# Performance work log

Hardware: AMD Instinct MI355X
Metric: run time of the kernel (lower is better)

Reference implementation:

```python
import jax, jax.numpy as jnp
import numpy as np

B, L, DIM, NH = 2, 2048, 1024, 16
HD = DIM // NH

def setup_inputs() -> dict:
    key = jax.random.key(0)
    ks = jax.random.split(key, 7)
    s = 1.0 / np.sqrt(DIM)
    x = jax.random.normal(ks[0], (B, L, DIM), dtype=jnp.float32)
    pos_bias = jax.random.normal(ks[1], (B, NH, L, L), dtype=jnp.float32)
    mask = jax.random.randint(ks[2], (B, L), 0, 2, dtype=jnp.int32)
    wq = jax.random.normal(ks[3], (DIM, DIM), dtype=jnp.float32) * s
    wk = jax.random.normal(ks[4], (DIM, DIM), dtype=jnp.float32) * s
    wv = jax.random.normal(ks[5], (DIM, DIM), dtype=jnp.float32) * s
    wo = jax.random.normal(ks[6], (DIM, DIM), dtype=jnp.float32) * s
    return {"x": x, "pos_bias": pos_bias, "mask": mask, "wq": wq, "wk": wk, "wv": wv, "wo": wo}

def reference(x, pos_bias, mask, wq, wk, wv, wo):
    b, l, _ = x.shape
    # projections (bias-free linears); reshape to [B, L, n, c]
    q = (x @ wq).reshape(b, l, NH, HD)
    k = (x @ wk).reshape(b, l, NH, HD)
    v = (x @ wv).reshape(b, l, NH, HD)
    # additive bias: pos_bias, with masked positions set to dtype min (T5: no 1/sqrt(d) scaling)
    neg = jnp.finfo(x.dtype).min
    attn_bias = jnp.where(mask[:, None, None, :] == 0, neg, pos_bias)
    scores = jnp.einsum('binc,bjnc->bnij', q, k) + attn_bias  # [B, n, L, L]
    attn = jax.nn.softmax(scores, axis=-1)
    out = jnp.einsum('bnij,bjnc->binc', attn, v).reshape(b, l, DIM)
    return out @ wo
```

## Files before the change

### kernel.cpp

```cpp
#include <hip/hip_runtime.h>
#include <cmath>

typedef _Float16 half8 __attribute__((ext_vector_type(8)));
typedef _Float16 half4 __attribute__((ext_vector_type(4)));
typedef float f32x4 __attribute__((ext_vector_type(4)));

#define NEGBIG (-3.4028235e38f)

__global__ void cast4_kernel(const float* __restrict__ in, _Float16* __restrict__ out, int n) {
    int i = (blockIdx.x * 256 + threadIdx.x) * 4;
    if (i < n) {
        float4 v = *(const float4*)&in[i];
        half4 o = { (_Float16)v.x, (_Float16)v.y, (_Float16)v.z, (_Float16)v.w };
        *(half4*)&out[i] = o;
    }
}

__global__ void transpose_cast_kernel(const float* __restrict__ W, _Float16* __restrict__ Wt) {
    __shared__ float tile[32][33];
    int bx = blockIdx.x * 32;
    int by = blockIdx.y * 32;
    int tx = threadIdx.x & 31, ty = threadIdx.x >> 5;
    #pragma unroll
    for (int r = 0; r < 32; r += 8)
        tile[ty + r][tx] = W[(size_t)(bx + ty + r) * 1024 + by + tx];
    __syncthreads();
    #pragma unroll
    for (int r = 0; r < 32; r += 8)
        Wt[(size_t)(by + ty + r) * 1024 + bx + tx] = (_Float16)tile[tx][ty + r];
}

__global__ __launch_bounds__(256)
void gemm_qkv_kernel(const _Float16* __restrict__ X,
                     const _Float16* __restrict__ WqT, const _Float16* __restrict__ WkT,
                     const _Float16* __restrict__ WvT,
                     _Float16* __restrict__ Qh, _Float16* __restrict__ Kh, _Float16* __restrict__ VTh)
{
    const int z = blockIdx.z;
    const _Float16* __restrict__ Bt = (z == 0) ? WqT : (z == 1) ? WkT : WvT;
    _Float16* __restrict__ out      = (z == 0) ? Qh  : (z == 1) ? Kh  : VTh;

    __shared__ _Float16 Asb[128][40];
    __shared__ _Float16 Bsb[128][40];

    const int tid = threadIdx.x;
    const int bm = blockIdx.x * 128;
    const int bn = blockIdx.y * 128;
    const int wave = tid >> 6, lane = tid & 63;
    const int wm = (wave >> 1) * 64, wn = (wave & 1) * 64;
    const int quad = lane >> 4, l16 = lane & 15;

    f32x4 acc[4][4] = {};

    for (int k0 = 0; k0 < 1024; k0 += 32) {
        #pragma unroll
        for (int c = 0; c < 2; ++c) {
            int chunk = tid + c * 256;
            int row = chunk >> 2;
            int kc  = (chunk & 3) * 8;
            *(half8*)&Asb[row][kc] = *(const half8*)&X [(size_t)(bm + row) * 1024 + k0 + kc];
            *(half8*)&Bsb[row][kc] = *(const half8*)&Bt[(size_t)(bn + row) * 1024 + k0 + kc];
        }
        __syncthreads();
        half8 af[4], bf[4];
        #pragma unroll
        for (int mt = 0; mt < 4; ++mt) af[mt] = *(const half8*)&Asb[wm + mt*16 + l16][quad * 8];
        #pragma unroll
        for (int nt = 0; nt < 4; ++nt) bf[nt] = *(const half8*)&Bsb[wn + nt*16 + l16][quad * 8];
        if (z == 2) {
            #pragma unroll
            for (int mt = 0; mt < 4; ++mt)
                #pragma unroll
                for (int nt = 0; nt < 4; ++nt)
                    acc[mt][nt] = __builtin_amdgcn_mfma_f32_16x16x32_f16(bf[nt], af[mt], acc[mt][nt], 0, 0, 0);
        } else {
            #pragma unroll
            for (int mt = 0; mt < 4; ++mt)
                #pragma unroll
                for (int nt = 0; nt < 4; ++nt)
                    acc[mt][nt] = __builtin_amdgcn_mfma_f32_16x16x32_f16(af[mt], bf[nt], acc[mt][nt], 0, 0, 0);
        }
        __syncthreads();
    }

    if (z < 2) {
        #pragma unroll
        for (int mt = 0; mt < 4; ++mt) {
            #pragma unroll
            for (int nt = 0; nt < 4; ++nt) {
                #pragma unroll
                for (int r = 0; r < 4; ++r) {
                    int m = bm + wm + mt * 16 + quad * 4 + r;
                    int n = bn + wn + nt * 16 + l16;
                    _Float16 hv = (_Float16)acc[mt][nt][r];
                    int bb = m >> 11, ll = m & 2047, hh = n >> 6, dd = n & 63;
                    out[(((size_t)(bb * 16 + hh)) * 2048 + ll) * 64 + dd] = hv;
                }
            }
        }
    } else {
        #pragma unroll
        for (int mt = 0; mt < 4; ++mt) {
            #pragma unroll
            for (int nt = 0; nt < 4; ++nt) {
                #pragma unroll
                for (int r = 0; r < 4; ++r) {
                    int n = bn + wn + nt * 16 + quad * 4 + r;
                    int m = bm + wm + mt * 16 + l16;
                    _Float16 hv = (_Float16)acc[mt][nt][r];
                    int bb = m >> 11, ll = m & 2047, hh = n >> 6, dd = n & 63;
                    out[(((size_t)(bb * 16 + hh)) * 64 + dd) * 2048 + ll] = hv;
                }
            }
        }
    }
}

__device__ __forceinline__ float rowmax16(float v) {
    #pragma unroll
    for (int off = 1; off < 16; off <<= 1) v = fmaxf(v, __shfl_xor(v, off));
    return v;
}
__device__ __forceinline__ float rowsum16(float v) {
    #pragma unroll
    for (int off = 1; off < 16; off <<= 1) v += __shfl_xor(v, off);
    return v;
}

__global__ __launch_bounds__(256)
void flash_attn_kernel(const _Float16* __restrict__ Qh, const _Float16* __restrict__ Kh,
                       const _Float16* __restrict__ VTh, const float* __restrict__ bias,
                       const int* __restrict__ mask, _Float16* __restrict__ AO)
{
    const int qt = blockIdx.x, h = blockIdx.y, b = blockIdx.z;
    const int tid = threadIdx.x, wave = tid >> 6, lane = tid & 63;
    const int quad = lane >> 4, l16 = lane & 15;

    __shared__ _Float16 Kt[64][72];
    __shared__ _Float16 Vt[64][72];
    __shared__ float    Bs[64][68];
    __shared__ _Float16 Pw[4][16][72];

    const size_t head = (size_t)(b * 16 + h) * 2048 * 64;
    const int i_base = qt * 64 + wave * 16;
    const float* __restrict__ bias_base = bias + ((size_t)((b * 16 + h) * 2048 + qt * 64)) * 2048;
    const int* __restrict__ mask_base = mask + b * 2048;

    half8 qf0 = *(const half8*)&Qh[head + (size_t)(i_base + l16) * 64 + quad * 8];
    half8 qf1 = *(const half8*)&Qh[head + (size_t)(i_base + l16) * 64 + 32 + quad * 8];

    float m_r[4] = { -INFINITY, -INFINITY, -INFINITY, -INFINITY };
    float l_r[4] = {};
    f32x4 o[4] = {};

    const int kv_row = tid >> 3;
    const int kv_dc  = (tid & 7) * 8;
    const int b_row0 = tid >> 4;
    const int b_col  = (tid & 15) * 4;

    half8 kreg[2], vreg[2];
    f32x4 breg[4];
    int4  mreg;

    auto prefetch = [&](int j0) {
        #pragma unroll
        for (int c = 0; c < 2; ++c) {
            int row = kv_row + c * 32;
            kreg[c] = *(const half8*)&Kh [head + (size_t)(j0 + row) * 64 + kv_dc];
            vreg[c] = *(const half8*)&VTh[head + (size_t)row * 2048 + j0 + kv_dc];
        }
        mreg = *(const int4*)&mask_base[j0 + b_col];
        #pragma unroll
        for (int c = 0; c < 4; ++c)
            breg[c] = *(const f32x4*)&bias_base[(size_t)(b_row0 + c * 16) * 2048 + j0 + b_col];
    };

    prefetch(0);

    for (int j0 = 0; j0 < 2048; j0 += 64) {
        #pragma unroll
        for (int c = 0; c < 2; ++c) {
            int row = kv_row + c * 32;
            *(half8*)&Kt[row][kv_dc] = kreg[c];
            *(half8*)&Vt[row][kv_dc] = vreg[c];
        }
        #pragma unroll
        for (int c = 0; c < 4; ++c) {
            float* dst = &Bs[b_row0 + c * 16][b_col];
            dst[0] = mreg.x ? breg[c][0] : NEGBIG;
            dst[1] = mreg.y ? breg[c][1] : NEGBIG;
            dst[2] = mreg.z ? breg[c][2] : NEGBIG;
            dst[3] = mreg.w ? breg[c][3] : NEGBIG;
        }
        __syncthreads();

        if (j0 + 64 < 2048) prefetch(j0 + 64);

        const int iw = wave * 16 + quad * 4;
        float sreg[4][4];
        #pragma unroll
        for (int jt = 0; jt < 4; ++jt) {
            half8 kf0 = *(const half8*)&Kt[jt * 16 + l16][quad * 8];
            half8 kf1 = *(const half8*)&Kt[jt * 16 + l16][32 + quad * 8];
            f32x4 s = {};
            __builtin_amdgcn_s_setprio(1);
            s = __builtin_amdgcn_mfma_f32_16x16x32_f16(qf0, kf0, s, 0, 0, 0);
            s = __builtin_amdgcn_mfma_f32_16x16x32_f16(qf1, kf1, s, 0, 0, 0);
            __builtin_amdgcn_s_setprio(0);
            #pragma unroll
            for (int r = 0; r < 4; ++r)
                sreg[jt][r] = s[r] + Bs[iw + r][jt * 16 + l16];
        }

        float alpha[4];
        #pragma unroll
        for (int r = 0; r < 4; ++r) {
            float mx = fmaxf(fmaxf(sreg[0][r], sreg[1][r]), fmaxf(sreg[2][r], sreg[3][r]));
            mx = rowmax16(mx);
            float mnew = fmaxf(m_r[r], mx);
            alpha[r] = __expf(m_r[r] - mnew);
            m_r[r] = mnew;
            float ps = 0.f;
            #pragma unroll
            for (int jt = 0; jt < 4; ++jt) {
                float p = __expf(sreg[jt][r] - mnew);
                Pw[wave][quad * 4 + r][jt * 16 + l16] = (_Float16)p;
                ps += p;
            }
            ps = rowsum16(ps);
            l_r[r] = l_r[r] * alpha[r] + ps;
        }
        #pragma unroll
        for (int nt = 0; nt < 4; ++nt)
            #pragma unroll
            for (int r = 0; r < 4; ++r)
                o[nt][r] *= alpha[r];

        half8 pf0 = *(const half8*)&Pw[wave][l16][quad * 8];
        half8 pf1 = *(const half8*)&Pw[wave][l16][32 + quad * 8];
        #pragma unroll
        for (int nt = 0; nt < 4; ++nt) {
            half8 vf0 = *(const half8*)&Vt[nt * 16 + l16][quad * 8];
            half8 vf1 = *(const half8*)&Vt[nt * 16 + l16][32 + quad * 8];
            __builtin_amdgcn_s_setprio(1);
            o[nt] = __builtin_amdgcn_mfma_f32_16x16x32_f16(pf0, vf0, o[nt], 0, 0, 0);
            o[nt] = __builtin_amdgcn_mfma_f32_16x16x32_f16(pf1, vf1, o[nt], 0, 0, 0);
            __builtin_amdgcn_s_setprio(0);
        }
        __syncthreads();
    }

    #pragma unroll
    for (int nt = 0; nt < 4; ++nt) {
        #pragma unroll
        for (int r = 0; r < 4; ++r) {
            float val = o[nt][r] / l_r[r];
            AO[(size_t)(b * 2048 + i_base + quad * 4 + r) * 1024 + h * 64 + nt * 16 + l16] = (_Float16)val;
        }
    }
}

__global__ __launch_bounds__(256)
void gemm_out_kernel(const _Float16* __restrict__ A, const _Float16* __restrict__ Bt,
                     float* __restrict__ C)
{
    __shared__ _Float16 Asb[128][40];
    __shared__ _Float16 Bsb[128][40];

    const int tid = threadIdx.x;
    const int bm = blockIdx.x * 128;
    const int bn = blockIdx.y * 128;
    const int wave = tid >> 6, lane = tid & 63;
    const int wm = (wave >> 1) * 64, wn = (wave & 1) * 64;
    const int quad = lane >> 4, l16 = lane & 15;

    f32x4 acc[4][4] = {};

    for (int k0 = 0; k0 < 1024; k0 += 32) {
        #pragma unroll
        for (int c = 0; c < 2; ++c) {
            int chunk = tid + c * 256;
            int row = chunk >> 2;
            int kc  = (chunk & 3) * 8;
            *(half8*)&Asb[row][kc] = *(const half8*)&A [(size_t)(bm + row) * 1024 + k0 + kc];
            *(half8*)&Bsb[row][kc] = *(const half8*)&Bt[(size_t)(bn + row) * 1024 + k0 + kc];
        }
        __syncthreads();
        half8 af[4], bf[4];
        #pragma unroll
        for (int mt = 0; mt < 4; ++mt) af[mt] = *(const half8*)&Asb[wm + mt*16 + l16][quad * 8];
        #pragma unroll
        for (int nt = 0; nt < 4; ++nt) bf[nt] = *(const half8*)&Bsb[wn + nt*16 + l16][quad * 8];
        #pragma unroll
        for (int mt = 0; mt < 4; ++mt)
            #pragma unroll
            for (int nt = 0; nt < 4; ++nt)
                acc[mt][nt] = __builtin_amdgcn_mfma_f32_16x16x32_f16(af[mt], bf[nt], acc[mt][nt], 0, 0, 0);
        __syncthreads();
    }

    #pragma unroll
    for (int mt = 0; mt < 4; ++mt)
        #pragma unroll
        for (int nt = 0; nt < 4; ++nt)
            #pragma unroll
            for (int r = 0; r < 4; ++r) {
                int m = bm + wm + mt * 16 + quad * 4 + r;
                int n = bn + wn + nt * 16 + l16;
                C[(size_t)m * 1024 + n] = acc[mt][nt][r];
            }
}

extern "C" void kernel_launch(void* const* d_in, const int* in_sizes, int n_in,
                              void* d_out, int out_size, void* d_ws, size_t ws_size,
                              hipStream_t stream)
{
    const float* x    = (const float*)d_in[0];
    const float* bias = (const float*)d_in[1];
    const int*   mask = (const int*)d_in[2];
    const float* wq   = (const float*)d_in[3];
    const float* wk   = (const float*)d_in[4];
    const float* wv   = (const float*)d_in[5];
    const float* wo   = (const float*)d_in[6];
    float* out = (float*)d_out;

    char* ws = (char*)d_ws;
    const size_t MB = 1024 * 1024;
    _Float16* x_h = (_Float16*)(ws + 0);
    _Float16* AO  = x_h;
    _Float16* wqT = (_Float16*)(ws + 8 * MB);
    _Float16* wkT = (_Float16*)(ws + 10 * MB);
    _Float16* wvT = (_Float16*)(ws + 12 * MB);
    _Float16* woT = (_Float16*)(ws + 14 * MB);
    _Float16* Qh  = (_Float16*)(ws + 16 * MB);
    _Float16* Kh  = (_Float16*)(ws + 24 * MB);
    _Float16* VTh = (_Float16*)(ws + 32 * MB);

    cast4_kernel<<<4096, 256, 0, stream>>>(x, x_h, 4096 * 1024);
    dim3 tg(32, 32);
    transpose_cast_kernel<<<tg, 256, 0, stream>>>(wq, wqT);
    transpose_cast_kernel<<<tg, 256, 0, stream>>>(wk, wkT);
    transpose_cast_kernel<<<tg, 256, 0, stream>>>(wv, wvT);
    transpose_cast_kernel<<<tg, 256, 0, stream>>>(wo, woT);

    gemm_qkv_kernel<<<dim3(32, 8, 3), 256, 0, stream>>>(x_h, wqT, wkT, wvT, Qh, Kh, VTh);
    flash_attn_kernel<<<dim3(32, 16, 2), 256, 0, stream>>>(Qh, Kh, VTh, bias, mask, AO);
    gemm_out_kernel<<<dim3(32, 8), 256, 0, stream>>>(AO, woT, out);
}
```

Baseline: 846.4 us.

## Transpose attention MFMA layout, read bias in registers, use direct-to-LDS GEMM loads

The attention kernel swaps the MFMA operand order so each lane holds one query row's scores. Bias and mask are then loaded straight into registers instead of being staged through shared memory, and the row max and sum reductions shrink to two cross-lane shuffles. Both GEMMs now use global_load_lds to copy tiles directly into unpadded shared memory, and the four weight transpose launches are merged into one. The unpadded LDS tiles may cause bank conflicts, and the GEMM loop still synchronizes on every tile without double buffering.

```diff
diff --git a/kernel.cpp b/kernel.cpp
--- a/kernel.cpp
+++ b/kernel.cpp
@@ -6,6 +6,11 @@
 typedef float f32x4 __attribute__((ext_vector_type(4)));
 
 #define NEGBIG (-3.4028235e38f)
+
+__device__ __forceinline__ void gload16(void* lds, const void* g) {
+    __builtin_amdgcn_global_load_lds((const __attribute__((address_space(1))) void*)g,
+                                     (__attribute__((address_space(3))) void*)lds, 16, 0, 0);
+}
 
 __global__ void cast4_kernel(const float* __restrict__ in, _Float16* __restrict__ out, int n) {
     int i = (blockIdx.x * 256 + threadIdx.x) * 4;
@@ -16,7 +21,13 @@
     }
 }
 
-__global__ void transpose_cast_kernel(const float* __restrict__ W, _Float16* __restrict__ Wt) {
+__global__ void transpose_cast_kernel(const float* __restrict__ W0, const float* __restrict__ W1,
+                                      const float* __restrict__ W2, const float* __restrict__ W3,
+                                      _Float16* __restrict__ T0, _Float16* __restrict__ T1,
+                                      _Float16* __restrict__ T2, _Float16* __restrict__ T3) {
+    const int z = blockIdx.z;
+    const float* __restrict__ W = (z == 0) ? W0 : (z == 1) ? W1 : (z == 2) ? W2 : W3;
+    _Float16* __restrict__ Wt   = (z == 0) ? T0 : (z == 1) ? T1 : (z == 2) ? T2 : T3;
     __shared__ float tile[32][33];
     int bx = blockIdx.x * 32;
     int by = blockIdx.y * 32;
@@ -40,8 +51,8 @@
     const _Float16* __restrict__ Bt = (z == 0) ? WqT : (z == 1) ? WkT : WvT;
     _Float16* __restrict__ out      = (z == 0) ? Qh  : (z == 1) ? Kh  : VTh;
 
-    __shared__ _Float16 Asb[128][40];
-    __shared__ _Float16 Bsb[128][40];
+    __shared__ __align__(16) _Float16 As[128][32];
+    __shared__ __align__(16) _Float16 Bs[128][32];
 
     const int tid = threadIdx.x;
     const int bm = blockIdx.x * 128;
@@ -50,23 +61,25 @@
     const int wm = (wave >> 1) * 64, wn = (wave & 1) * 64;
     const int quad = lane >> 4, l16 = lane & 15;
 
+    const int srow = wave * 32 + (lane >> 2);
+    const int scol = (lane & 3) * 8;
+    const _Float16* gA = &X [(size_t)(bm + srow) * 1024 + scol];
+    const _Float16* gB = &Bt[(size_t)(bn + srow) * 1024 + scol];
+
     f32x4 acc[4][4] = {};
 
     for (int k0 = 0; k0 < 1024; k0 += 32) {
-        #pragma unroll
-        for (int c = 0; c < 2; ++c) {
-            int chunk = tid + c * 256;
-            int row = chunk >> 2;
-            int kc  = (chunk & 3) * 8;
-            *(half8*)&Asb[row][kc] = *(const half8*)&X [(size_t)(bm + row) * 1024 + k0 + kc];
-            *(half8*)&Bsb[row][kc] = *(const half8*)&Bt[(size_t)(bn + row) * 1024 + k0 + kc];
-        }
-        __syncthreads();
+        gload16(&As[wave * 32][0],      gA + k0);
+        gload16(&As[wave * 32 + 16][0], gA + 16 * 1024 + k0);
+        gload16(&Bs[wave * 32][0],      gB + k0);
+        gload16(&Bs[wave * 32 + 16][0], gB + 16 * 1024 + k0);
+        __syncthreads();
+
         half8 af[4], bf[4];
         #pragma unroll
-        for (int mt = 0; mt < 4; ++mt) af[mt] = *(const half8*)&Asb[wm + mt*16 + l16][quad * 8];
-        #pragma unroll
-        for (int nt = 0; nt < 4; ++nt) bf[nt] = *(const half8*)&Bsb[wn + nt*16 + l16][quad * 8];
+        for (int mt = 0; mt < 4; ++mt) af[mt] = *(const half8*)&As[wm + mt*16 + l16][quad * 8];
+        #pragma unroll
+        for (int nt = 0; nt < 4; ++nt) bf[nt] = *(const half8*)&Bs[wn + nt*16 + l16][quad * 8];
         if (z == 2) {
             #pragma unroll
             for (int mt = 0; mt < 4; ++mt)
@@ -116,17 +129,6 @@
     }
 }
 
-__device__ __forceinline__ float rowmax16(float v) {
-    #pragma unroll
-    for (int off = 1; off < 16; off <<= 1) v = fmaxf(v, __shfl_xor(v, off));
-    return v;
-}
-__device__ __forceinline__ float rowsum16(float v) {
-    #pragma unroll
-    for (int off = 1; off < 16; off <<= 1) v += __shfl_xor(v, off);
-    return v;
-}
-
 __global__ __launch_bounds__(256)
 void flash_attn_kernel(const _Float16* __restrict__ Qh, const _Float16* __restrict__ Kh,
                        const _Float16* __restrict__ VTh, const float* __restrict__ bias,
@@ -138,44 +140,45 @@
 
     __shared__ _Float16 Kt[64][72];
     __shared__ _Float16 Vt[64][72];
-    __shared__ float    Bs[64][68];
     __shared__ _Float16 Pw[4][16][72];
 
     const size_t head = (size_t)(b * 16 + h) * 2048 * 64;
     const int i_base = qt * 64 + wave * 16;
-    const float* __restrict__ bias_base = bias + ((size_t)((b * 16 + h) * 2048 + qt * 64)) * 2048;
+    const int qrow = i_base + l16;
+    const float* __restrict__ bias_row = bias + ((size_t)((b * 16 + h) * 2048 + qrow)) * 2048;
     const int* __restrict__ mask_base = mask + b * 2048;
 
-    half8 qf0 = *(const half8*)&Qh[head + (size_t)(i_base + l16) * 64 + quad * 8];
-    half8 qf1 = *(const half8*)&Qh[head + (size_t)(i_base + l16) * 64 + 32 + quad * 8];
-
-    float m_r[4] = { -INFINITY, -INFINITY, -INFINITY, -INFINITY };
-    float l_r[4] = {};
+    half8 qf0 = *(const half8*)&Qh[head + (size_t)qrow * 64 + quad * 8];
+    half8 qf1 = *(const half8*)&Qh[head + (size_t)qrow * 64 + 32 + quad * 8];
+
+    float m_r = -INFINITY, l_r = 0.f;
     f32x4 o[4] = {};
 
     const int kv_row = tid >> 3;
     const int kv_dc  = (tid & 7) * 8;
-    const int b_row0 = tid >> 4;
-    const int b_col  = (tid & 15) * 4;
 
     half8 kreg[2], vreg[2];
     f32x4 breg[4];
-    int4  mreg;
-
-    auto prefetch = [&](int j0) {
+    int4  mreg[4];
+
+    auto prefetchKV = [&](int j0) {
         #pragma unroll
         for (int c = 0; c < 2; ++c) {
             int row = kv_row + c * 32;
             kreg[c] = *(const half8*)&Kh [head + (size_t)(j0 + row) * 64 + kv_dc];
             vreg[c] = *(const half8*)&VTh[head + (size_t)row * 2048 + j0 + kv_dc];
         }
-        mreg = *(const int4*)&mask_base[j0 + b_col];
-        #pragma unroll
-        for (int c = 0; c < 4; ++c)
-            breg[c] = *(const f32x4*)&bias_base[(size_t)(b_row0 + c * 16) * 2048 + j0 + b_col];
     };
-
-    prefetch(0);
+    auto prefetchB = [&](int j0) {
+        #pragma unroll
+        for (int jt = 0; jt < 4; ++jt) {
+            breg[jt] = *(const f32x4*)&bias_row [j0 + jt * 16 + quad * 4];
+            mreg[jt] = *(const int4*) &mask_base[j0 + jt * 16 + quad * 4];
+        }
+    };
+
+    prefetchKV(0);
+    prefetchB(0);
 
     for (int j0 = 0; j0 < 2048; j0 += 64) {
         #pragma unroll
@@ -184,57 +187,51 @@
             *(half8*)&Kt[row][kv_dc] = kreg[c];
             *(half8*)&Vt[row][kv_dc] = vreg[c];
         }
-        #pragma unroll
-        for (int c = 0; c < 4; ++c) {
-            float* dst = &Bs[b_row0 + c * 16][b_col];
-            dst[0] = mreg.x ? breg[c][0] : NEGBIG;
-            dst[1] = mreg.y ? breg[c][1] : NEGBIG;
-            dst[2] = mreg.z ? breg[c][2] : NEGBIG;
-            dst[3] = mreg.w ? breg[c][3] : NEGBIG;
-        }
-        __syncthreads();
-
-        if (j0 + 64 < 2048) prefetch(j0 + 64);
-
-        const int iw = wave * 16 + quad * 4;
-        float sreg[4][4];
+        __syncthreads();
+        if (j0 + 64 < 2048) prefetchKV(j0 + 64);
+
+        float sreg[16];
         #pragma unroll
         for (int jt = 0; jt < 4; ++jt) {
             half8 kf0 = *(const half8*)&Kt[jt * 16 + l16][quad * 8];
             half8 kf1 = *(const half8*)&Kt[jt * 16 + l16][32 + quad * 8];
             f32x4 s = {};
             __builtin_amdgcn_s_setprio(1);
-            s = __builtin_amdgcn_mfma_f32_16x16x32_f16(qf0, kf0, s, 0, 0, 0);
-            s = __builtin_amdgcn_mfma_f32_16x16x32_f16(qf1, kf1, s, 0, 0, 0);
+            s = __builtin_amdgcn_mfma_f32_16x16x32_f16(kf0, qf0, s, 0, 0, 0);
+            s = __builtin_amdgcn_mfma_f32_16x16x32_f16(kf1, qf1, s, 0, 0, 0);
             __builtin_amdgcn_s_setprio(0);
-            #pragma unroll
-            for (int r = 0; r < 4; ++r)
-                sreg[jt][r] = s[r] + Bs[iw + r][jt * 16 + l16];
-        }
-
-        float alpha[4];
-        #pragma unroll
-        for (int r = 0; r < 4; ++r) {
-            float mx = fmaxf(fmaxf(sreg[0][r], sreg[1][r]), fmaxf(sreg[2][r], sreg[3][r]));
-            mx = rowmax16(mx);
-            float mnew = fmaxf(m_r[r], mx);
-            alpha[r] = __expf(m_r[r] - mnew);
-            m_r[r] = mnew;
-            float ps = 0.f;
-            #pragma unroll
-            for (int jt = 0; jt < 4; ++jt) {
-                float p = __expf(sreg[jt][r] - mnew);
-                Pw[wave][quad * 4 + r][jt * 16 + l16] = (_Float16)p;
-                ps += p;
-            }
-            ps = rowsum16(ps);
-            l_r[r] = l_r[r] * alpha[r] + ps;
-        }
-        #pragma unroll
-        for (int nt = 0; nt < 4; ++nt)
-            #pragma unroll
-            for (int r = 0; r < 4; ++r)
-                o[nt][r] *= alpha[r];
+            sreg[jt*4+0] = mreg[jt].x ? (s[0] + breg[jt][0]) : NEGBIG;
+            sreg[jt*4+1] = mreg[jt].y ? (s[1] + breg[jt][1]) : NEGBIG;
+            sreg[jt*4+2] = mreg[jt].z ? (s[2] + breg[jt][2]) : NEGBIG;
+            sreg[jt*4+3] = mreg[jt].w ? (s[3] + breg[jt][3]) : NEGBIG;
+        }
+        if (j0 + 64 < 2048) prefetchB(j0 + 64);
+
+        float mx = sreg[0];
+        #pragma unroll
+        for (int i = 1; i < 16; ++i) mx = fmaxf(mx, sreg[i]);
+        mx = fmaxf(mx, __shfl_xor(mx, 16));
+        mx = fmaxf(mx, __shfl_xor(mx, 32));
+        float mnew = fmaxf(m_r, mx);
+        float alpha = __expf(m_r - mnew);
+        m_r = mnew;
+
+        float p[16], ps = 0.f;
+        #pragma unroll
+        for (int i = 0; i < 16; ++i) { p[i] = __expf(sreg[i] - mnew); ps += p[i]; }
+        #pragma unroll
+        for (int jt = 0; jt < 4; ++jt) {
+            half4 pk = { (_Float16)p[jt*4], (_Float16)p[jt*4+1],
+                         (_Float16)p[jt*4+2], (_Float16)p[jt*4+3] };
+            *(half4*)&Pw[wave][l16][jt * 16 + quad * 4] = pk;
+        }
+        ps += __shfl_xor(ps, 16);
+        ps += __shfl_xor(ps, 32);
+        l_r = l_r * alpha + ps;
+        #pragma unroll
+        for (int nt = 0; nt < 4; ++nt) {
+            o[nt][0] *= alpha; o[nt][1] *= alpha; o[nt][2] *= alpha; o[nt][3] *= alpha;
+        }
 
         half8 pf0 = *(const half8*)&Pw[wave][l16][quad * 8];
         half8 pf1 = *(const half8*)&Pw[wave][l16][32 + quad * 8];
@@ -243,20 +240,19 @@
             half8 vf0 = *(const half8*)&Vt[nt * 16 + l16][quad * 8];
             half8 vf1 = *(const half8*)&Vt[nt * 16 + l16][32 + quad * 8];
             __builtin_amdgcn_s_setprio(1);
-            o[nt] = __builtin_amdgcn_mfma_f32_16x16x32_f16(pf0, vf0, o[nt], 0, 0, 0);
-            o[nt] = __builtin_amdgcn_mfma_f32_16x16x32_f16(pf1, vf1, o[nt], 0, 0, 0);
+            o[nt] = __builtin_amdgcn_mfma_f32_16x16x32_f16(vf0, pf0, o[nt], 0, 0, 0);
+            o[nt] = __builtin_amdgcn_mfma_f32_16x16x32_f16(vf1, pf1, o[nt], 0, 0, 0);
             __builtin_amdgcn_s_setprio(0);
         }
         __syncthreads();
     }
 
+    const float inv = 1.0f / l_r;
     #pragma unroll
     for (int nt = 0; nt < 4; ++nt) {
-        #pragma unroll
-        for (int r = 0; r < 4; ++r) {
-            float val = o[nt][r] / l_r[r];
-            AO[(size_t)(b * 2048 + i_base + quad * 4 + r) * 1024 + h * 64 + nt * 16 + l16] = (_Float16)val;
-        }
+        half4 ov = { (_Float16)(o[nt][0] * inv), (_Float16)(o[nt][1] * inv),
+                     (_Float16)(o[nt][2] * inv), (_Float16)(o[nt][3] * inv) };
+        *(half4*)&AO[(size_t)(b * 2048 + qrow) * 1024 + h * 64 + nt * 16 + quad * 4] = ov;
     }
 }
 
@@ -264,8 +260,8 @@
 void gemm_out_kernel(const _Float16* __restrict__ A, const _Float16* __restrict__ Bt,
                      float* __restrict__ C)
 {
-    __shared__ _Float16 Asb[128][40];
-    __shared__ _Float16 Bsb[128][40];
+    __shared__ __align__(16) _Float16 As[128][32];
+    __shared__ __align__(16) _Float16 Bs[128][32];
 
     const int tid = threadIdx.x;
     const int bm = blockIdx.x * 128;
@@ -274,23 +270,25 @@
     const int wm = (wave >> 1) * 64, wn = (wave & 1) * 64;
     const int quad = lane >> 4, l16 = lane & 15;
 
+    const int srow = wave * 32 + (lane >> 2);
+    const int scol = (lane & 3) * 8;
+    const _Float16* gA = &A [(size_t)(bm + srow) * 1024 + scol];
+    const _Float16* gB = &Bt[(size_t)(bn + srow) * 1024 + scol];
+
     f32x4 acc[4][4] = {};
 
     for (int k0 = 0; k0 < 1024; k0 += 32) {
-        #pragma unroll
-        for (int c = 0; c < 2; ++c) {
-            int chunk = tid + c * 256;
-            int row = chunk >> 2;
-            int kc  = (chunk & 3) * 8;
-            *(half8*)&Asb[row][kc] = *(const half8*)&A [(size_t)(bm + row) * 1024 + k0 + kc];
-            *(half8*)&Bsb[row][kc] = *(const half8*)&Bt[(size_t)(bn + row) * 1024 + k0 + kc];
-        }
-        __syncthreads();
+        gload16(&As[wave * 32][0],      gA + k0);
+        gload16(&As[wave * 32 + 16][0], gA + 16 * 1024 + k0);
+        gload16(&Bs[wave * 32][0],      gB + k0);
+        gload16(&Bs[wave * 32 + 16][0], gB + 16 * 1024 + k0);
+        __syncthreads();
+
         half8 af[4], bf[4];
         #pragma unroll
-        for (int mt = 0; mt < 4; ++mt) af[mt] = *(const half8*)&Asb[wm + mt*16 + l16][quad * 8];
-        #pragma unroll
-        for (int nt = 0; nt < 4; ++nt) bf[nt] = *(const half8*)&Bsb[wn + nt*16 + l16][quad * 8];
+        for (int mt = 0; mt < 4; ++mt) af[mt] = *(const half8*)&As[wm + mt*16 + l16][quad * 8];
+        #pragma unroll
+        for (int nt = 0; nt < 4; ++nt) bf[nt] = *(const half8*)&Bs[wn + nt*16 + l16][quad * 8];
         #pragma unroll
         for (int mt = 0; mt < 4; ++mt)
             #pragma unroll
@@ -337,11 +335,7 @@
     _Float16* VTh = (_Float16*)(ws + 32 * MB);
 
     cast4_kernel<<<4096, 256, 0, stream>>>(x, x_h, 4096 * 1024);
-    dim3 tg(32, 32);
-    transpose_cast_kernel<<<tg, 256, 0, stream>>>(wq, wqT);
-    transpose_cast_kernel<<<tg, 256, 0, stream>>>(wk, wkT);
-    transpose_cast_kernel<<<tg, 256, 0, stream>>>(wv, wvT);
-    transpose_cast_kernel<<<tg, 256, 0, stream>>>(wo, woT);
+    transpose_cast_kernel<<<dim3(32, 32, 4), 256, 0, stream>>>(wq, wk, wv, wo, wqT, wkT, wvT, woT);
 
     gemm_qkv_kernel<<<dim3(32, 8, 3), 256, 0, stream>>>(x_h, wqT, wkT, wvT, Qh, Kh, VTh);
     flash_attn_kernel<<<dim3(32, 16, 2), 256, 0, stream>>>(Qh, Kh, VTh, bias, mask, AO);
```

After: 850.7 us. Within noise of the previous version (+0.5%).
